# Kernel optimization log

Measured on AMD Instinct MI355X. Metric: run time of the kernel, lower is better.

## Reference

```python
import jax, jax.numpy as jnp
import numpy as np

B, N, C = 8, 1024, 1024
H = 16
D = C // H  # head_dim = 64
SCALE = D ** -0.5


def setup_inputs() -> dict:
    key = jax.random.key(0)
    k1, k2, k3 = jax.random.split(key, 3)
    x = jax.random.normal(k1, (B, N, C), dtype=jnp.float32)
    w_qkv = jax.random.normal(k2, (3 * C, C), dtype=jnp.float32) * (C ** -0.5)
    w_proj = jax.random.normal(k3, (C, C), dtype=jnp.float32) * (C ** -0.5)
    b_proj = jnp.zeros((C,), dtype=jnp.float32)
    return {"x": x, "w_qkv": w_qkv, "w_proj": w_proj, "b_proj": b_proj}


def reference(x, w_qkv, w_proj, b_proj):
    Bx, Nx, Cx = x.shape
    # qkv: [B,N,3C] -> [3,B,H,N,D]
    qkv = jnp.einsum('bnc,oc->bno', x, w_qkv)
    qkv = qkv.reshape(Bx, Nx, 3, H, D).transpose(2, 0, 3, 1, 4)
    q, k, v = qkv[0], qkv[1], qkv[2]
    attn = jnp.einsum('bhnd,bhmd->bhnm', q, k) * SCALE  # [B,H,N,N]
    attn = jax.nn.softmax(attn, axis=-1)
    out = jnp.einsum('bhnm,bhmd->bhnd', attn, v)  # [B,H,N,D]
    out = out.transpose(0, 2, 1, 3).reshape(Bx, Nx, Cx)
    return jnp.einsum('bnc,oc->bno', out, w_proj) + b_proj
```

## Files before the change

kernel.cpp:

```cpp
#include <hip/hip_runtime.h>

typedef _Float16 half8 __attribute__((ext_vector_type(8)));
typedef _Float16 half4v __attribute__((ext_vector_type(4)));
typedef _Float16 half2v __attribute__((ext_vector_type(2)));
typedef float floatx4 __attribute__((ext_vector_type(4)));

#define AS3 __attribute__((address_space(3)))
#define AS1 __attribute__((address_space(1)))

__device__ __forceinline__ void gload_lds16(const _Float16* g, _Float16* l) {
    __builtin_amdgcn_global_load_lds((AS1 void*)g, (AS3 void*)l, 16, 0, 0);
}

__global__ __launch_bounds__(256) void cvt_all(const float* __restrict__ x,
                                               const float* __restrict__ wq,
                                               const float* __restrict__ wp,
                                               _Float16* __restrict__ xh,
                                               _Float16* __restrict__ wqh,
                                               _Float16* __restrict__ wph) {
    long i = (long)blockIdx.x * 256 + threadIdx.x;
    const float4* src; half4v* dst; long off;
    if (i < 2097152)      { src = (const float4*)x;  dst = (half4v*)xh;  off = i; }
    else if (i < 2883584) { src = (const float4*)wq; dst = (half4v*)wqh; off = i - 2097152; }
    else                  { src = (const float4*)wp; dst = (half4v*)wph; off = i - 2883584; }
    float4 v = src[off];
    half4v h = {(_Float16)v.x, (_Float16)v.y, (_Float16)v.z, (_Float16)v.w};
    dst[off] = h;
}

__global__ __launch_bounds__(256, 4) void gemm_tn(
    const _Float16* __restrict__ A, const _Float16* __restrict__ B,
    _Float16* __restrict__ Ch, int ldc, _Float16* __restrict__ Vt, int split,
    float* __restrict__ Cf, const float* __restrict__ bias,
    int M, int Nn, int K)
{
    __shared__ _Float16 sA[2][128 * 32];
    __shared__ _Float16 sB[2][128 * 32];
    const int tid  = threadIdx.x;
    const int lane = tid & 63, wave = tid >> 6;
    const int quad = lane >> 4, l16 = lane & 15;
    const int wr = wave >> 1, wc = wave & 1;
    const long m0 = (long)blockIdx.x * 128, n0 = (long)blockIdx.y * 128;

    const int srow = tid >> 2;
    const int csw = ((tid & 3) ^ ((srow >> 1) & 3)) * 8;
    const _Float16* gA0 = A + (m0 + srow) * (long)K + csw;
    const _Float16* gA1 = A + (m0 + srow + 64) * (long)K + csw;
    const _Float16* gB0 = B + (n0 + srow) * (long)K + csw;
    const _Float16* gB1 = B + (n0 + srow + 64) * (long)K + csw;
    const int wbase = wave << 4;

#define STAGE(bf, koff)                                                  \
    do {                                                                 \
        gload_lds16(gA0 + (koff), &sA[bf][wbase * 32]);                  \
        gload_lds16(gA1 + (koff), &sA[bf][(wbase + 64) * 32]);           \
        gload_lds16(gB0 + (koff), &sB[bf][wbase * 32]);                  \
        gload_lds16(gB1 + (koff), &sB[bf][(wbase + 64) * 32]);           \
    } while (0)

    const int swz = (l16 >> 1) & 3;
    const int aoff = ((quad ^ swz) * 8);

    floatx4 acc[4][4] = {};
    const int nk = K >> 5;

    STAGE(0, 0);

    for (int kk = 0; kk < nk; kk++) {
        const int cur = kk & 1;
        __syncthreads();
        if (kk + 1 < nk)
            STAGE(cur ^ 1, (long)(kk + 1) << 5);

        const _Float16* cA = &sA[cur][0];
        const _Float16* cB = &sB[cur][0];
        half8 af[4], bf[4];
#pragma unroll
        for (int t = 0; t < 4; t++)
            af[t] = *(const half8*)&cA[(wr * 64 + t * 16 + l16) * 32 + aoff];
#pragma unroll
        for (int t = 0; t < 4; t++)
            bf[t] = *(const half8*)&cB[(wc * 64 + t * 16 + l16) * 32 + aoff];
#pragma unroll
        for (int tm = 0; tm < 4; tm++)
#pragma unroll
            for (int tn = 0; tn < 4; tn++)
                acc[tm][tn] = __builtin_amdgcn_mfma_f32_16x16x32_f16(af[tm], bf[tn], acc[tm][tn], 0, 0, 0);
    }
#undef STAGE

#pragma unroll
    for (int tm = 0; tm < 4; tm++) {
        long row = m0 + wr * 64 + tm * 16 + quad * 4;
#pragma unroll
        for (int tn = 0; tn < 4; tn++) {
            long col = n0 + wc * 64 + tn * 16 + l16;
            if (Cf) {
                float bv = bias ? bias[col] : 0.f;
#pragma unroll
                for (int r = 0; r < 4; r++)
                    Cf[(row + r) * (long)Nn + col] = acc[tm][tn][r] + bv;
            } else if (col >= split) {
                long cv = col - split;
                long vrow = ((row >> 10) * 16 + (cv >> 6)) * 64 + (cv & 63);
                long nn = row & 1023;
                half4v pv = {(_Float16)acc[tm][tn][0], (_Float16)acc[tm][tn][1],
                             (_Float16)acc[tm][tn][2], (_Float16)acc[tm][tn][3]};
                *(half4v*)&Vt[vrow * 1024 + nn] = pv;
            } else {
#pragma unroll
                for (int r = 0; r < 4; r++)
                    Ch[(row + r) * (long)ldc + col] = (_Float16)acc[tm][tn][r];
            }
        }
    }
}

#define CSC 0.125f
__global__ __launch_bounds__(256, 4) void flash_attn(const _Float16* __restrict__ qk,
                                                     const _Float16* __restrict__ vt,
                                                     _Float16* __restrict__ out)
{
    const int bh = blockIdx.x, b = bh >> 4, h = bh & 15;
    const int n0 = blockIdx.y * 128;
    const int tid = threadIdx.x, lane = tid & 63, wave = tid >> 6;
    const int quad = lane >> 4, l16 = lane & 15;

    __shared__ _Float16 sK[64 * 72];
    __shared__ _Float16 sVT[64 * 72];
    __shared__ _Float16 sPT[4][32 * 72];

    half8 qf[2][2];
    const _Float16* qbase = qk + (long)(b * 1024 + n0 + wave * 32) * 2048 + h * 64;
#pragma unroll
    for (int t = 0; t < 2; t++)
#pragma unroll
        for (int s = 0; s < 2; s++)
            qf[t][s] = *(const half8*)(qbase + (long)(t * 16 + l16) * 2048 + s * 32 + quad * 8);

    const int srow = tid >> 3, scol8 = (tid & 7) * 8;
    const _Float16* kgb = qk + 1024 + h * 64 + scol8 + (long)(b * 1024 + srow) * 2048;
    const _Float16* vgb = vt + (long)(bh * 64 + srow) * 1024 + scol8;

    float m_[2] = {-1e30f, -1e30f}, l_[2] = {0.f, 0.f};
    floatx4 o[2][4] = {};

    for (int kt = 0; kt < 16; kt++) {
        const int kr0 = kt * 64;
        __syncthreads();
#pragma unroll
        for (int i = 0; i < 2; i++) {
            int r = srow + i * 32;
            *(half8*)&sK[r * 72 + scol8]  = *(const half8*)(kgb + (long)(kr0 + i * 32) * 2048);
            *(half8*)&sVT[r * 72 + scol8] = *(const half8*)(vgb + (long)(i * 32) * 1024 + kr0);
        }
        __syncthreads();

        floatx4 sacc[2][4] = {};
#pragma unroll
        for (int c = 0; c < 4; c++)
#pragma unroll
            for (int s = 0; s < 2; s++) {
                half8 kf = *(const half8*)&sK[(c * 16 + l16) * 72 + s * 32 + quad * 8];
                sacc[0][c] = __builtin_amdgcn_mfma_f32_16x16x32_f16(kf, qf[0][s], sacc[0][c], 0, 0, 0);
                sacc[1][c] = __builtin_amdgcn_mfma_f32_16x16x32_f16(kf, qf[1][s], sacc[1][c], 0, 0, 0);
            }

#pragma unroll
        for (int t = 0; t < 2; t++) {
            float mx = -1e30f;
#pragma unroll
            for (int c = 0; c < 4; c++)
#pragma unroll
                for (int r = 0; r < 4; r++) {
                    float v = sacc[t][c][r] * CSC;
                    sacc[t][c][r] = v;
                    mx = fmaxf(mx, v);
                }
            mx = fmaxf(mx, __shfl_xor(mx, 16));
            mx = fmaxf(mx, __shfl_xor(mx, 32));
            float mn = fmaxf(m_[t], mx);
            float al = __expf(m_[t] - mn);
            m_[t] = mn;
            float rs = 0.f;
#pragma unroll
            for (int c = 0; c < 4; c++)
#pragma unroll
                for (int r = 0; r < 4; r++) {
                    float p = __expf(sacc[t][c][r] - mn);
                    sacc[t][c][r] = p;
                    rs += p;
                }
            rs += __shfl_xor(rs, 16);
            rs += __shfl_xor(rs, 32);
            l_[t] = l_[t] * al + rs;
#pragma unroll
            for (int dt = 0; dt < 4; dt++) o[t][dt] *= al;
#pragma unroll
            for (int c = 0; c < 4; c++) {
                half4v p = {(_Float16)sacc[t][c][0], (_Float16)sacc[t][c][1],
                            (_Float16)sacc[t][c][2], (_Float16)sacc[t][c][3]};
                *(half4v*)&sPT[wave][(t * 16 + l16) * 72 + c * 16 + quad * 4] = p;
            }
        }

#pragma unroll
        for (int kk = 0; kk < 2; kk++) {
            half8 pf0 = *(const half8*)&sPT[wave][(l16) * 72 + kk * 32 + quad * 8];
            half8 pf1 = *(const half8*)&sPT[wave][(16 + l16) * 72 + kk * 32 + quad * 8];
#pragma unroll
            for (int dt = 0; dt < 4; dt++) {
                half8 vf = *(const half8*)&sVT[(dt * 16 + l16) * 72 + kk * 32 + quad * 8];
                o[0][dt] = __builtin_amdgcn_mfma_f32_16x16x32_f16(vf, pf0, o[0][dt], 0, 0, 0);
                o[1][dt] = __builtin_amdgcn_mfma_f32_16x16x32_f16(vf, pf1, o[1][dt], 0, 0, 0);
            }
        }
    }

#pragma unroll
    for (int t = 0; t < 2; t++) {
        float inv = 1.f / l_[t];
#pragma unroll
        for (int dt = 0; dt < 4; dt++) {
            floatx4 v = o[t][dt];
            half4v a = {(_Float16)(v[0] * inv), (_Float16)(v[1] * inv),
                        (_Float16)(v[2] * inv), (_Float16)(v[3] * inv)};
            *(half4v*)&sPT[wave][(t * 16 + l16) * 72 + dt * 16 + quad * 4] = a;
        }
    }
    __syncthreads();
#pragma unroll
    for (int i = 0; i < 4; i++) {
        int ql = i * 8 + (lane >> 3);
        int c8 = (lane & 7) * 8;
        half8 vv = *(const half8*)&sPT[wave][ql * 72 + c8];
        *(half8*)(out + (long)(b * 1024 + n0 + wave * 32 + ql) * 1024 + h * 64 + c8) = vv;
    }
}

extern "C" void kernel_launch(void* const* d_in, const int* in_sizes, int n_in,
                              void* d_out, int out_size, void* d_ws, size_t ws_size,
                              hipStream_t stream) {
    const float* x      = (const float*)d_in[0];
    const float* w_qkv  = (const float*)d_in[1];
    const float* w_proj = (const float*)d_in[2];
    const float* b_proj = (const float*)d_in[3];

    char* ws = (char*)d_ws;
    _Float16* qkh    = (_Float16*)ws;
    _Float16* vT     = (_Float16*)(ws + 33554432);
    _Float16* xh     = (_Float16*)(ws + 50331648);
    _Float16* wqkvh  = (_Float16*)(ws + 67108864);
    _Float16* wprojh = (_Float16*)(ws + 73400320);
    _Float16* attnh  = xh;

    cvt_all<<<12288, 256, 0, stream>>>(x, w_qkv, w_proj, xh, wqkvh, wprojh);

    gemm_tn<<<dim3(64, 24), 256, 0, stream>>>(xh, wqkvh, qkh, 2048, vT, 2048,
                                              nullptr, nullptr, 8192, 3072, 1024);
    flash_attn<<<dim3(128, 8), 256, 0, stream>>>(qkh, vT, attnh);
    gemm_tn<<<dim3(64, 8), 256, 0, stream>>>(attnh, wprojh, nullptr, 0, nullptr, 1 << 30,
                                             (float*)d_out, b_proj, 8192, 1024, 1024);
}
```

Measured before the change: 243.7 us.

## Add 256x256-tile QKV GEMM with 8 waves, XCD swizzle and interleaved staging

Replaces the 128x128 QKV projection GEMM with a new kernel that uses 256x256 tiles, 512 threads, BK=64 and a double-buffered LDS pipeline. The pipeline interleaves global-to-LDS loads with four MFMA phases, uses setprio around the MFMA blocks, and remaps block IDs so neighbouring tiles land on the same XCD. The larger tile raises arithmetic intensity and cuts global reloads. In exchange it uses 128KB of LDS per block, more accumulator registers, and a grid of only 384 blocks, which may underfill the GPU.

```diff
diff --git a/kernel.cpp b/kernel.cpp
--- a/kernel.cpp
+++ b/kernel.cpp
@@ -10,6 +10,10 @@
 
 __device__ __forceinline__ void gload_lds16(const _Float16* g, _Float16* l) {
     __builtin_amdgcn_global_load_lds((AS1 void*)g, (AS3 void*)l, 16, 0, 0);
+}
+
+__device__ __forceinline__ floatx4 mfma16(half8 a, half8 b, floatx4 c) {
+    return __builtin_amdgcn_mfma_f32_16x16x32_f16(a, b, c, 0, 0, 0);
 }
 
 __global__ __launch_bounds__(256) void cvt_all(const float* __restrict__ x,
@@ -28,6 +32,170 @@
     dst[off] = h;
 }
 
+__global__ __launch_bounds__(512, 2) void gemm256_qkv(
+    const _Float16* __restrict__ A, const _Float16* __restrict__ B,
+    _Float16* __restrict__ Ch, int ldc, _Float16* __restrict__ Vt, int split,
+    int K)
+{
+    __shared__ _Float16 sA[2 * 2 * 8192];
+    __shared__ _Float16 sB[2 * 2 * 8192];
+
+    const int nwg = gridDim.x * gridDim.y;
+    int bid = blockIdx.y * gridDim.x + blockIdx.x;
+    const int cpx = nwg >> 3;
+    bid = (bid & 7) * cpx + (bid >> 3);
+    const int bx = bid % gridDim.x, by = bid / gridDim.x;
+
+    const int tid = threadIdx.x;
+    const int lane = tid & 63, wave = tid >> 6;
+    const int quad = lane >> 4, l16 = lane & 15;
+    const int wm = wave >> 2, wn = wave & 3;
+    const int hB = wn >> 1;
+    const long m0 = (long)bx * 256, n0 = (long)by * 256;
+
+    const int gch = ((tid & 7) ^ ((tid >> 3) & 7)) * 8;
+    const _Float16* gA = A + (m0 + (tid >> 3)) * (long)K + gch;
+    const _Float16* gB = B + (n0 + (tid >> 3)) * (long)K + gch;
+    const int wst = wave * 512;
+
+#define STG_A(h, u) do {                                                          \
+    gload_lds16(gA + ((h) * 128L) * K + (u) * 64,                                 \
+                &sA[((u) & 1) * 16384 + (h) * 8192 + wst]);                       \
+    gload_lds16(gA + ((h) * 128L + 64) * K + (u) * 64,                            \
+                &sA[((u) & 1) * 16384 + (h) * 8192 + 4096 + wst]);                \
+} while (0)
+#define STG_B(h, u) do {                                                          \
+    gload_lds16(gB + ((h) * 128L) * K + (u) * 64,                                 \
+                &sB[((u) & 1) * 16384 + (h) * 8192 + wst]);                       \
+    gload_lds16(gB + ((h) * 128L + 64) * K + (u) * 64,                            \
+                &sB[((u) & 1) * 16384 + (h) * 8192 + 4096 + wst]);                \
+} while (0)
+
+    const int NT = K >> 6;
+    STG_A(0, 0); STG_B(0, 0); STG_B(1, 0); STG_A(1, 0);
+    STG_B(0, 1); STG_B(1, 1); STG_A(0, 1);
+    asm volatile("s_waitcnt vmcnt(6)" ::: "memory");
+    __builtin_amdgcn_s_barrier();
+
+    const int cs0 = (quad ^ (l16 & 7)) * 8;
+    const int cs1 = ((4 + quad) ^ (l16 & 7)) * 8;
+
+    floatx4 acc[8][4] = {};
+    half8 afr[4][2], b0[2][2], b1[2][2];
+
+    for (int t = 0; t < NT; ++t) {
+        const int cur = (t & 1) * 16384;
+        const _Float16* cA = &sA[cur + wm * 8192];
+        const _Float16* cB = &sB[cur + hB * 8192];
+
+#pragma unroll
+        for (int f = 0; f < 4; f++) {
+            const _Float16* p = &cA[(f * 16 + l16) * 64];
+            afr[f][0] = *(const half8*)&p[cs0];
+            afr[f][1] = *(const half8*)&p[cs1];
+        }
+#pragma unroll
+        for (int nf = 0; nf < 2; nf++) {
+            const _Float16* p = &cB[((wn & 1) * 64 + nf * 16 + l16) * 64];
+            b0[nf][0] = *(const half8*)&p[cs0];
+            b0[nf][1] = *(const half8*)&p[cs1];
+        }
+        if (t + 1 < NT) STG_A(1, t + 1);
+        __builtin_amdgcn_s_barrier();
+        asm volatile("s_waitcnt lgkmcnt(0)" ::: "memory");
+        __builtin_amdgcn_sched_barrier(0);
+        __builtin_amdgcn_s_setprio(1);
+#pragma unroll
+        for (int f = 0; f < 4; f++)
+#pragma unroll
+            for (int nf = 0; nf < 2; nf++) {
+                acc[f][nf] = mfma16(afr[f][0], b0[nf][0], acc[f][nf]);
+                acc[f][nf] = mfma16(afr[f][1], b0[nf][1], acc[f][nf]);
+            }
+        __builtin_amdgcn_s_setprio(0);
+        __builtin_amdgcn_s_barrier();
+
+#pragma unroll
+        for (int nf = 0; nf < 2; nf++) {
+            const _Float16* p = &cB[((wn & 1) * 64 + 32 + nf * 16 + l16) * 64];
+            b1[nf][0] = *(const half8*)&p[cs0];
+            b1[nf][1] = *(const half8*)&p[cs1];
+        }
+        __builtin_amdgcn_s_barrier();
+        asm volatile("s_waitcnt lgkmcnt(0)" ::: "memory");
+        __builtin_amdgcn_sched_barrier(0);
+        __builtin_amdgcn_s_setprio(1);
+#pragma unroll
+        for (int f = 0; f < 4; f++)
+#pragma unroll
+            for (int nf = 0; nf < 2; nf++) {
+                acc[f][2 + nf] = mfma16(afr[f][0], b1[nf][0], acc[f][2 + nf]);
+                acc[f][2 + nf] = mfma16(afr[f][1], b1[nf][1], acc[f][2 + nf]);
+            }
+        __builtin_amdgcn_s_setprio(0);
+        __builtin_amdgcn_s_barrier();
+
+#pragma unroll
+        for (int f = 0; f < 4; f++) {
+            const _Float16* p = &cA[(64 + f * 16 + l16) * 64];
+            afr[f][0] = *(const half8*)&p[cs0];
+            afr[f][1] = *(const half8*)&p[cs1];
+        }
+        if (t + 2 < NT) STG_B(0, t + 2);
+        __builtin_amdgcn_s_barrier();
+        asm volatile("s_waitcnt lgkmcnt(0)" ::: "memory");
+        __builtin_amdgcn_sched_barrier(0);
+        __builtin_amdgcn_s_setprio(1);
+#pragma unroll
+        for (int f = 0; f < 4; f++)
+#pragma unroll
+            for (int nf = 0; nf < 2; nf++) {
+                acc[4 + f][2 + nf] = mfma16(afr[f][0], b1[nf][0], acc[4 + f][2 + nf]);
+                acc[4 + f][2 + nf] = mfma16(afr[f][1], b1[nf][1], acc[4 + f][2 + nf]);
+            }
+        __builtin_amdgcn_s_setprio(0);
+        __builtin_amdgcn_s_barrier();
+
+        if (t + 2 < NT) { STG_B(1, t + 2); STG_A(0, t + 2); }
+        __builtin_amdgcn_s_barrier();
+        __builtin_amdgcn_s_setprio(1);
+#pragma unroll
+        for (int f = 0; f < 4; f++)
+#pragma unroll
+            for (int nf = 0; nf < 2; nf++) {
+                acc[4 + f][nf] = mfma16(afr[f][0], b0[nf][0], acc[4 + f][nf]);
+                acc[4 + f][nf] = mfma16(afr[f][1], b0[nf][1], acc[4 + f][nf]);
+            }
+        __builtin_amdgcn_s_setprio(0);
+        if (t < NT - 2)       { asm volatile("s_waitcnt vmcnt(6)" ::: "memory"); }
+        else if (t == NT - 2) { asm volatile("s_waitcnt vmcnt(0)" ::: "memory"); }
+        __builtin_amdgcn_s_barrier();
+    }
+#undef STG_A
+#undef STG_B
+
+#pragma unroll
+    for (int mf = 0; mf < 8; mf++) {
+        long row = m0 + wm * 128 + mf * 16 + quad * 4;
+#pragma unroll
+        for (int cn = 0; cn < 4; cn++) {
+            long col = n0 + wn * 64 + cn * 16 + l16;
+            if (col >= split) {
+                long cv = col - split;
+                long vrow = ((row >> 10) * 16 + (cv >> 6)) * 64 + (cv & 63);
+                long nn = row & 1023;
+                half4v pv = {(_Float16)acc[mf][cn][0], (_Float16)acc[mf][cn][1],
+                             (_Float16)acc[mf][cn][2], (_Float16)acc[mf][cn][3]};
+                *(half4v*)&Vt[vrow * 1024 + nn] = pv;
+            } else {
+#pragma unroll
+                for (int r = 0; r < 4; r++)
+                    Ch[(row + r) * (long)ldc + col] = (_Float16)acc[mf][cn][r];
+            }
+        }
+    }
+}
+
 __global__ __launch_bounds__(256, 4) void gemm_tn(
     const _Float16* __restrict__ A, const _Float16* __restrict__ B,
     _Float16* __restrict__ Ch, int ldc, _Float16* __restrict__ Vt, int split,
@@ -256,8 +424,7 @@
 
     cvt_all<<<12288, 256, 0, stream>>>(x, w_qkv, w_proj, xh, wqkvh, wprojh);
 
-    gemm_tn<<<dim3(64, 24), 256, 0, stream>>>(xh, wqkvh, qkh, 2048, vT, 2048,
-                                              nullptr, nullptr, 8192, 3072, 1024);
+    gemm256_qkv<<<dim3(32, 12), 512, 0, stream>>>(xh, wqkvh, qkh, 2048, vT, 2048, 1024);
     flash_attn<<<dim3(128, 8), 256, 0, stream>>>(qkh, vT, attnh);
     gemm_tn<<<dim3(64, 8), 256, 0, stream>>>(attnh, wprojh, nullptr, 0, nullptr, 1 << 30,
                                              (float*)d_out, b_proj, 8192, 1024, 1024);
```

After: 251.8 us. +3.3%, slower.

## Rewrite GEMM as 256x128 tile with triple-buffered LDS and XCD-aware block remap

Applied to the files above, without the earlier changes.

Replaces the 128x128 double-buffered GEMM with a 512-thread kernel using 256x128 tiles, a K-step of 64, and a three-stage LDS ring filled by async global-to-LDS loads. It interleaves LDS fragment reads with MFMA phases under explicit waitcnt, barrier and setprio control. Block IDs are remapped across the 8 XCDs and grouped for L2 locality. The aim is to hide load latency and raise data reuse in both projection GEMMs, at the cost of 144KB of LDS per block, lower occupancy and fragile manual synchronisation.

```diff
diff --git a/kernel.cpp b/kernel.cpp
--- a/kernel.cpp
+++ b/kernel.cpp
@@ -10,6 +10,10 @@
 
 __device__ __forceinline__ void gload_lds16(const _Float16* g, _Float16* l) {
     __builtin_amdgcn_global_load_lds((AS1 void*)g, (AS3 void*)l, 16, 0, 0);
+}
+
+__device__ __forceinline__ floatx4 mfma16(half8 a, half8 b, floatx4 c) {
+    return __builtin_amdgcn_mfma_f32_16x16x32_f16(a, b, c, 0, 0, 0);
 }
 
 __global__ __launch_bounds__(256) void cvt_all(const float* __restrict__ x,
@@ -28,89 +32,136 @@
     dst[off] = h;
 }
 
-__global__ __launch_bounds__(256, 4) void gemm_tn(
+__global__ __launch_bounds__(512, 2) void gemm256(
     const _Float16* __restrict__ A, const _Float16* __restrict__ B,
     _Float16* __restrict__ Ch, int ldc, _Float16* __restrict__ Vt, int split,
-    float* __restrict__ Cf, const float* __restrict__ bias,
-    int M, int Nn, int K)
+    float* __restrict__ Cf, const float* __restrict__ bias, int Nn, int K)
 {
-    __shared__ _Float16 sA[2][128 * 32];
-    __shared__ _Float16 sB[2][128 * 32];
-    const int tid  = threadIdx.x;
+    __shared__ _Float16 sAB[3 * 24576];
+
+    const int nwg = gridDim.x * gridDim.y;
+    int bid = blockIdx.y * gridDim.x + blockIdx.x;
+    const int cpx = nwg >> 3;
+    bid = (bid & 7) * cpx + (bid >> 3);
+    const int gsz = gridDim.y << 3;
+    const int bxg = bid / gsz;
+    const int rem = bid - bxg * gsz;
+    const int by = rem >> 3;
+    const int bx = (bxg << 3) + (rem & 7);
+
+    const int tid = threadIdx.x;
     const int lane = tid & 63, wave = tid >> 6;
     const int quad = lane >> 4, l16 = lane & 15;
-    const int wr = wave >> 1, wc = wave & 1;
-    const long m0 = (long)blockIdx.x * 128, n0 = (long)blockIdx.y * 128;
-
-    const int srow = tid >> 2;
-    const int csw = ((tid & 3) ^ ((srow >> 1) & 3)) * 8;
-    const _Float16* gA0 = A + (m0 + srow) * (long)K + csw;
-    const _Float16* gA1 = A + (m0 + srow + 64) * (long)K + csw;
-    const _Float16* gB0 = B + (n0 + srow) * (long)K + csw;
-    const _Float16* gB1 = B + (n0 + srow + 64) * (long)K + csw;
-    const int wbase = wave << 4;
-
-#define STAGE(bf, koff)                                                  \
-    do {                                                                 \
-        gload_lds16(gA0 + (koff), &sA[bf][wbase * 32]);                  \
-        gload_lds16(gA1 + (koff), &sA[bf][(wbase + 64) * 32]);           \
-        gload_lds16(gB0 + (koff), &sB[bf][wbase * 32]);                  \
-        gload_lds16(gB1 + (koff), &sB[bf][(wbase + 64) * 32]);           \
-    } while (0)
-
-    const int swz = (l16 >> 1) & 3;
-    const int aoff = ((quad ^ swz) * 8);
+    const int wm = wave >> 1, wn = wave & 1;
+    const long m0 = (long)bx * 256, n0 = (long)by * 128;
+
+    const int gch = ((tid & 7) ^ ((tid >> 3) & 7)) * 8;
+    const _Float16* gA = A + (m0 + (tid >> 3)) * (long)K + gch;
+    const _Float16* gB = B + (n0 + (tid >> 3)) * (long)K + gch;
+    const int wst = wave * 512;
+
+#define STAGE(sb, u) do {                                                     \
+    const long ko = (long)(u) * 64;                                           \
+    _Float16* d = &sAB[(sb) * 24576];                                         \
+    gload_lds16(gA + ko,                 d + wst);                            \
+    gload_lds16(gA +  64 * (long)K + ko, d + 4096  + wst);                    \
+    gload_lds16(gA + 128 * (long)K + ko, d + 8192  + wst);                    \
+    gload_lds16(gA + 192 * (long)K + ko, d + 12288 + wst);                    \
+    gload_lds16(gB + ko,                 d + 16384 + wst);                    \
+    gload_lds16(gB +  64 * (long)K + ko, d + 20480 + wst);                    \
+} while (0)
+
+    const int NT = K >> 6;
+    STAGE(0, 0); STAGE(1, 1);
+    asm volatile("s_waitcnt vmcnt(6)" ::: "memory");
+    __builtin_amdgcn_s_barrier();
+
+    const int cs0 = (quad ^ (l16 & 7)) * 8;
+    const int cs1 = ((4 + quad) ^ (l16 & 7)) * 8;
 
     floatx4 acc[4][4] = {};
-    const int nk = K >> 5;
-
-    STAGE(0, 0);
-
-    for (int kk = 0; kk < nk; kk++) {
-        const int cur = kk & 1;
-        __syncthreads();
-        if (kk + 1 < nk)
-            STAGE(cur ^ 1, (long)(kk + 1) << 5);
-
-        const _Float16* cA = &sA[cur][0];
-        const _Float16* cB = &sB[cur][0];
-        half8 af[4], bf[4];
-#pragma unroll
-        for (int t = 0; t < 4; t++)
-            af[t] = *(const half8*)&cA[(wr * 64 + t * 16 + l16) * 32 + aoff];
-#pragma unroll
-        for (int t = 0; t < 4; t++)
-            bf[t] = *(const half8*)&cB[(wc * 64 + t * 16 + l16) * 32 + aoff];
-#pragma unroll
-        for (int tm = 0; tm < 4; tm++)
-#pragma unroll
-            for (int tn = 0; tn < 4; tn++)
-                acc[tm][tn] = __builtin_amdgcn_mfma_f32_16x16x32_f16(af[tm], bf[tn], acc[tm][tn], 0, 0, 0);
+    half8 afr[4][2], bf0[2][2], bf1[2][2];
+
+    int cb = 0, sb = 2;
+    for (int t = 0; t < NT; ++t) {
+        const _Float16* cA = &sAB[cb * 24576 + wm * 4096];
+        const _Float16* cB = &sAB[cb * 24576 + 16384 + wn * 4096];
+
+#pragma unroll
+        for (int f = 0; f < 4; f++) {
+            const _Float16* p = &cA[(f * 16 + l16) * 64];
+            afr[f][0] = *(const half8*)&p[cs0];
+            afr[f][1] = *(const half8*)&p[cs1];
+        }
+#pragma unroll
+        for (int nf = 0; nf < 2; nf++) {
+            const _Float16* p = &cB[(nf * 16 + l16) * 64];
+            bf0[nf][0] = *(const half8*)&p[cs0];
+            bf0[nf][1] = *(const half8*)&p[cs1];
+        }
+        if (t + 2 < NT) STAGE(sb, t + 2);
+        __builtin_amdgcn_s_barrier();
+        asm volatile("s_waitcnt lgkmcnt(0)" ::: "memory");
+        __builtin_amdgcn_sched_barrier(0);
+        __builtin_amdgcn_s_setprio(1);
+#pragma unroll
+        for (int f = 0; f < 4; f++)
+#pragma unroll
+            for (int nf = 0; nf < 2; nf++) {
+                acc[f][nf] = mfma16(afr[f][0], bf0[nf][0], acc[f][nf]);
+                acc[f][nf] = mfma16(afr[f][1], bf0[nf][1], acc[f][nf]);
+            }
+        __builtin_amdgcn_s_setprio(0);
+        __builtin_amdgcn_s_barrier();
+
+#pragma unroll
+        for (int nf = 0; nf < 2; nf++) {
+            const _Float16* p = &cB[((2 + nf) * 16 + l16) * 64];
+            bf1[nf][0] = *(const half8*)&p[cs0];
+            bf1[nf][1] = *(const half8*)&p[cs1];
+        }
+        __builtin_amdgcn_s_barrier();
+        asm volatile("s_waitcnt lgkmcnt(0)" ::: "memory");
+        __builtin_amdgcn_sched_barrier(0);
+        __builtin_amdgcn_s_setprio(1);
+#pragma unroll
+        for (int f = 0; f < 4; f++)
+#pragma unroll
+            for (int nf = 0; nf < 2; nf++) {
+                acc[f][2 + nf] = mfma16(afr[f][0], bf1[nf][0], acc[f][2 + nf]);
+                acc[f][2 + nf] = mfma16(afr[f][1], bf1[nf][1], acc[f][2 + nf]);
+            }
+        __builtin_amdgcn_s_setprio(0);
+        if (t + 2 < NT)       { asm volatile("s_waitcnt vmcnt(6)" ::: "memory"); }
+        else if (t == NT - 2) { asm volatile("s_waitcnt vmcnt(0)" ::: "memory"); }
+        __builtin_amdgcn_s_barrier();
+        cb = (cb + 1 == 3) ? 0 : cb + 1;
+        sb = (sb + 1 == 3) ? 0 : sb + 1;
     }
 #undef STAGE
 
 #pragma unroll
-    for (int tm = 0; tm < 4; tm++) {
-        long row = m0 + wr * 64 + tm * 16 + quad * 4;
-#pragma unroll
-        for (int tn = 0; tn < 4; tn++) {
-            long col = n0 + wc * 64 + tn * 16 + l16;
+    for (int f = 0; f < 4; f++) {
+        long row = m0 + wm * 64 + f * 16 + quad * 4;
+#pragma unroll
+        for (int cn = 0; cn < 4; cn++) {
+            long col = n0 + wn * 64 + cn * 16 + l16;
             if (Cf) {
                 float bv = bias ? bias[col] : 0.f;
 #pragma unroll
                 for (int r = 0; r < 4; r++)
-                    Cf[(row + r) * (long)Nn + col] = acc[tm][tn][r] + bv;
+                    Cf[(row + r) * (long)Nn + col] = acc[f][cn][r] + bv;
             } else if (col >= split) {
                 long cv = col - split;
                 long vrow = ((row >> 10) * 16 + (cv >> 6)) * 64 + (cv & 63);
                 long nn = row & 1023;
-                half4v pv = {(_Float16)acc[tm][tn][0], (_Float16)acc[tm][tn][1],
-                             (_Float16)acc[tm][tn][2], (_Float16)acc[tm][tn][3]};
+                half4v pv = {(_Float16)acc[f][cn][0], (_Float16)acc[f][cn][1],
+                             (_Float16)acc[f][cn][2], (_Float16)acc[f][cn][3]};
                 *(half4v*)&Vt[vrow * 1024 + nn] = pv;
             } else {
 #pragma unroll
                 for (int r = 0; r < 4; r++)
-                    Ch[(row + r) * (long)ldc + col] = (_Float16)acc[tm][tn][r];
+                    Ch[(row + r) * (long)ldc + col] = (_Float16)acc[f][cn][r];
             }
         }
     }
@@ -256,9 +307,9 @@
 
     cvt_all<<<12288, 256, 0, stream>>>(x, w_qkv, w_proj, xh, wqkvh, wprojh);
 
-    gemm_tn<<<dim3(64, 24), 256, 0, stream>>>(xh, wqkvh, qkh, 2048, vT, 2048,
-                                              nullptr, nullptr, 8192, 3072, 1024);
+    gemm256<<<dim3(32, 24), 512, 0, stream>>>(xh, wqkvh, qkh, 2048, vT, 2048,
+                                              nullptr, nullptr, 3072, 1024);
     flash_attn<<<dim3(128, 8), 256, 0, stream>>>(qkh, vT, attnh);
-    gemm_tn<<<dim3(64, 8), 256, 0, stream>>>(attnh, wprojh, nullptr, 0, nullptr, 1 << 30,
-                                             (float*)d_out, b_proj, 8192, 1024, 1024);
-}
+    gemm256<<<dim3(32, 8), 512, 0, stream>>>(attnh, wprojh, nullptr, 0, nullptr, 1 << 30,
+                                             (float*)d_out, b_proj, 1024, 1024);
+}
```

New measurement: 236.1 us. 1.03x faster.
